# Performance work log

Measured on AMD Instinct MI355X. Metric: run time of the kernel, lower is better.

## Reference

```python
import jax, jax.numpy as jnp
import numpy as np

N_HEADS = 4
D_K = 64


def setup_inputs() -> dict:
    key = jax.random.key(0)
    k1, k2, k3, k4, k5 = jax.random.split(key, 5)
    C = 256
    return {
        "x": jax.random.normal(k1, (16, C, 32, 32), dtype=jnp.float32),
        "W_qkv": jax.random.normal(k2, (C, N_HEADS * D_K * 3), dtype=jnp.float32) * (C ** -0.5),
        "b_qkv": jax.random.normal(k3, (N_HEADS * D_K * 3,), dtype=jnp.float32) * 0.02,
        "W_out": jax.random.normal(k4, (N_HEADS * D_K, C), dtype=jnp.float32) * ((N_HEADS * D_K) ** -0.5),
        "b_out": jax.random.normal(k5, (C,), dtype=jnp.float32) * 0.02,
    }


def reference(x, W_qkv, b_qkv, W_out, b_out):
    # NOTE: the original forward never applies self.norm and ignores t.
    B, C, H, W = x.shape
    N = H * W
    scale = D_K ** -0.5
    xf = x.reshape(B, C, N).transpose(0, 2, 1)            # [B, N, C]
    qkv = (xf @ W_qkv + b_qkv).reshape(B, N, N_HEADS, 3 * D_K)
    q, k, v = jnp.split(qkv, 3, axis=-1)                  # each [B, N, H, dk]
    attn = jnp.einsum('bihd,bjhd->bijh', q, k) * scale    # [B, N, N, H]
    attn = jax.nn.softmax(attn, axis=2)                   # softmax over keys (j)
    res = jnp.einsum('bijh,bjhd->bihd', attn, v)          # [B, N, H, dk]
    res = res.reshape(B, N, N_HEADS * D_K)
    res = res @ W_out + b_out + xf                        # residual on flattened x
    return res.transpose(0, 2, 1).reshape(B, C, H, W)
```

## Files before the change

kernel.cpp:

```cpp
#include <hip/hip_runtime.h>
#include <math.h>

#define NN 1024

typedef __attribute__((ext_vector_type(8))) __bf16 bf16x8;
typedef __attribute__((ext_vector_type(4))) __bf16 bf16x4;
typedef __attribute__((ext_vector_type(4))) float f32x4;

__device__ __forceinline__ unsigned short f2bf(float f) {
    __bf16 h = (__bf16)f;
    return *(unsigned short*)&h;
}
__device__ __forceinline__ ushort4 pack4(float a, float b, float c, float d) {
    bf16x4 v;
    v[0] = (__bf16)a; v[1] = (__bf16)b; v[2] = (__bf16)c; v[3] = (__bf16)d;
    return *(ushort4*)&v;
}

__device__ __forceinline__ void async_cp16(const unsigned short* g, unsigned short* l) {
    __builtin_amdgcn_global_load_lds(
        (const __attribute__((address_space(1))) unsigned int*)g,
        (__attribute__((address_space(3))) unsigned int*)l,
        16, 0, 0);
}

__global__ __launch_bounds__(256) void prep_transpose(
    const float* __restrict__ x, const float* __restrict__ Wq,
    const float* __restrict__ Wo,
    unsigned short* __restrict__ xb, unsigned short* __restrict__ Wqt,
    unsigned short* __restrict__ Wot)
{
    __shared__ __align__(16) unsigned short T[64 * 72];
    const int bx = blockIdx.x;
    const int rt = blockIdx.y;
    const float* src; unsigned short* dst; int ncol, c0;
    if (bx < 256) {
        int b = bx >> 4; int ct = bx & 15;
        src = x + (size_t)b * 256 * 1024; dst = xb + (size_t)b * 1024 * 256;
        ncol = 1024; c0 = ct * 64;
    } else if (bx < 268) {
        src = Wq; dst = Wqt; ncol = 768; c0 = (bx - 256) * 64;
    } else {
        src = Wo; dst = Wot; ncol = 256; c0 = (bx - 268) * 64;
    }
    const int t = threadIdx.x;
    #pragma unroll
    for (int i = 0; i < 4; ++i) {
        int r  = i * 16 + (t >> 4);
        int c4 = (t & 15) * 4;
        float4 v = *(const float4*)&src[(size_t)(rt * 64 + r) * ncol + c0 + c4];
        *(ushort4*)&T[r * 72 + c4] = pack4(v.x, v.y, v.z, v.w);
    }
    __syncthreads();
    #pragma unroll
    for (int i = 0; i < 2; ++i) {
        int task = t + 256 * i;
        int c = task & 63, rs = task >> 6;
        ushort u8[8];
        #pragma unroll
        for (int k = 0; k < 8; ++k) u8[k] = T[(rs * 8 + k) * 72 + c];
        *(uint4*)&dst[(size_t)(c0 + c) * 256 + rt * 64 + rs * 8] = *(uint4*)u8;
    }
}

__global__ __launch_bounds__(256, 4) void qkv_gemm(
    const unsigned short* __restrict__ xb, const unsigned short* __restrict__ Wqt,
    const float* __restrict__ bias,
    unsigned short* __restrict__ Qb, unsigned short* __restrict__ Kb,
    unsigned short* __restrict__ Vtb)
{
    __shared__ __align__(16) unsigned short As[128 * 40];
    __shared__ __align__(16) unsigned short Bs[128 * 40];
    const int jt = blockIdx.x;
    const int m0 = blockIdx.y * 128;
    const int b  = m0 >> 10;
    const int n0 = m0 & 1023;
    const int t = threadIdx.x;
    const int w = t >> 6, lane = t & 63, quad = lane >> 4, cc = lane & 15;
    const int wm = (w & 1) * 64;
    const int wj = (w >> 1) * 64;

    f32x4 acc[4][4];
    #pragma unroll
    for (int ms = 0; ms < 4; ++ms)
        #pragma unroll
        for (int js = 0; js < 4; ++js) acc[ms][js] = (f32x4)(0.f);

    for (int k0 = 0; k0 < 256; k0 += 32) {
        __syncthreads();
        #pragma unroll
        for (int i = 0; i < 2; ++i) {
            int flat = t + 256 * i;
            int row = flat >> 2, seg = flat & 3;
            *(uint4*)&As[row * 40 + seg * 8] =
                *(const uint4*)&xb[(size_t)(m0 + row) * 256 + k0 + seg * 8];
            *(uint4*)&Bs[row * 40 + seg * 8] =
                *(const uint4*)&Wqt[(size_t)(jt * 128 + row) * 256 + k0 + seg * 8];
        }
        __syncthreads();
        bf16x8 af[4], bfr[4];
        #pragma unroll
        for (int ms = 0; ms < 4; ++ms)
            af[ms] = *(bf16x8*)&As[(wm + ms * 16 + cc) * 40 + quad * 8];
        #pragma unroll
        for (int js = 0; js < 4; ++js)
            bfr[js] = *(bf16x8*)&Bs[(wj + js * 16 + cc) * 40 + quad * 8];
        #pragma unroll
        for (int ms = 0; ms < 4; ++ms)
            #pragma unroll
            for (int js = 0; js < 4; ++js)
                acc[ms][js] = __builtin_amdgcn_mfma_f32_16x16x32_bf16(
                    af[ms], bfr[js], acc[ms][js], 0, 0, 0);
    }

    const int chunk = jt * 2 + (w >> 1);
    const int h = chunk / 3, type = chunk % 3;
    const size_t bh = (size_t)b * 4 + h;
    float bias_r[4];
    #pragma unroll
    for (int js = 0; js < 4; ++js) bias_r[js] = bias[jt * 128 + wj + js * 16 + cc];

    if (type == 2) {
        #pragma unroll
        for (int ms = 0; ms < 4; ++ms)
            #pragma unroll
            for (int js = 0; js < 4; ++js) {
                int dd = js * 16 + cc;
                int n = n0 + wm + ms * 16 + quad * 4;
                *(ushort4*)&Vtb[(bh * 64 + dd) * NN + n] =
                    pack4(acc[ms][js][0] + bias_r[js], acc[ms][js][1] + bias_r[js],
                          acc[ms][js][2] + bias_r[js], acc[ms][js][3] + bias_r[js]);
            }
    } else {
        unsigned short* dst = type ? Kb : Qb;
        const float sc = type ? 1.0f : 0.125f;
        #pragma unroll
        for (int ms = 0; ms < 4; ++ms)
            #pragma unroll
            for (int js = 0; js < 4; ++js)
                #pragma unroll
                for (int r = 0; r < 4; ++r) {
                    int n = n0 + wm + ms * 16 + quad * 4 + r;
                    dst[(bh * NN + n) * 64 + js * 16 + cc] =
                        f2bf((acc[ms][js][r] + bias_r[js]) * sc);
                }
    }
}

__global__ __launch_bounds__(256) void flash_attn(
    const unsigned short* __restrict__ Qb, const unsigned short* __restrict__ Kb,
    const unsigned short* __restrict__ Vtb, unsigned short* __restrict__ resb)
{
    __shared__ __align__(16) unsigned short Qs[4096];
    __shared__ __align__(16) unsigned short Ks0[4096];
    __shared__ __align__(16) unsigned short Ks1[4096];
    __shared__ __align__(16) unsigned short Vt0[4096];
    __shared__ __align__(16) unsigned short Vt1[4096];
    __shared__ __align__(16) unsigned short Ps[64 * 72];

    const int blk = blockIdx.x;
    const int qt = blk & 15;
    const int h  = (blk >> 4) & 3;
    const int b  = blk >> 6;
    const int t  = threadIdx.x;
    const int w  = t >> 6;
    const int lane = t & 63;
    const int quad = lane >> 4;
    const int c    = lane & 15;

    const size_t bh = (size_t)(b * 4 + h);
    const unsigned short* Qg = Qb  + bh * NN * 64;
    const unsigned short* Kg = Kb  + bh * NN * 64;
    const unsigned short* Vg = Vtb + bh * 64 * NN;

    #pragma unroll
    for (int i = 0; i < 2; ++i) {
        int f = i * 256 + t;
        int row = f >> 3;
        int gc  = (f & 7) ^ (row & 7);
        async_cp16(&Qg[(size_t)(qt * 64 + row) * 64 + gc * 8], &Qs[f * 8]);
        async_cp16(&Kg[(size_t)row * 64 + gc * 8], &Ks0[f * 8]);
        async_cp16(&Vg[(size_t)row * NN + gc * 8], &Vt0[f * 8]);
    }
    __syncthreads();

    bf16x8 qf[2];
    #pragma unroll
    for (int ks = 0; ks < 2; ++ks) {
        int sc_ = (ks * 4 + quad) ^ (c & 7);
        qf[ks] = *(bf16x8*)&Qs[((w * 16 + c) * 8 + sc_) * 8];
    }

    float m_i = -INFINITY, l_i = 0.f;
    f32x4 O[4];
    #pragma unroll
    for (int dt = 0; dt < 4; ++dt) O[dt] = (f32x4)(0.f);

    auto step = [&](int kt, const unsigned short* curK, const unsigned short* curV,
                    unsigned short* nxtK, unsigned short* nxtV,
                    bool pref, bool bar) {
        if (bar) __syncthreads();
        if (pref) {
            int ktn = kt + 1;
            #pragma unroll
            for (int i = 0; i < 2; ++i) {
                int f = i * 256 + t;
                int row = f >> 3;
                int gc  = (f & 7) ^ (row & 7);
                async_cp16(&Kg[(size_t)(ktn * 64 + row) * 64 + gc * 8], &nxtK[f * 8]);
                async_cp16(&Vg[(size_t)row * NN + ktn * 64 + gc * 8], &nxtV[f * 8]);
            }
        }

        f32x4 S[4];
        #pragma unroll
        for (int jt = 0; jt < 4; ++jt) S[jt] = (f32x4)(0.f);
        #pragma unroll
        for (int ks = 0; ks < 2; ++ks) {
            #pragma unroll
            for (int jt = 0; jt < 4; ++jt) {
                int sc_ = (ks * 4 + quad) ^ (c & 7);
                bf16x8 kf = *(bf16x8*)&curK[((jt * 16 + c) * 8 + sc_) * 8];
                S[jt] = __builtin_amdgcn_mfma_f32_16x16x32_bf16(kf, qf[ks], S[jt], 0, 0, 0);
            }
        }

        float mt = -INFINITY;
        #pragma unroll
        for (int jt = 0; jt < 4; ++jt)
            #pragma unroll
            for (int r = 0; r < 4; ++r) mt = fmaxf(mt, S[jt][r]);
        mt = fmaxf(mt, __shfl_xor(mt, 16));
        mt = fmaxf(mt, __shfl_xor(mt, 32));
        float mn = fmaxf(m_i, mt);
        float alpha = __expf(m_i - mn);
        float p[4][4];
        float rs = 0.f;
        #pragma unroll
        for (int jt = 0; jt < 4; ++jt)
            #pragma unroll
            for (int r = 0; r < 4; ++r) {
                p[jt][r] = __expf(S[jt][r] - mn);
                rs += p[jt][r];
            }
        rs += __shfl_xor(rs, 16);
        rs += __shfl_xor(rs, 32);
        l_i = l_i * alpha + rs;
        m_i = mn;

        #pragma unroll
        for (int jt = 0; jt < 4; ++jt)
            *(ushort4*)&Ps[(w * 16 + c) * 72 + jt * 16 + quad * 4] =
                pack4(p[jt][0], p[jt][1], p[jt][2], p[jt][3]);

        float alpha_r[4];
        #pragma unroll
        for (int r = 0; r < 4; ++r) alpha_r[r] = __shfl(alpha, quad * 4 + r);
        #pragma unroll
        for (int dt = 0; dt < 4; ++dt)
            #pragma unroll
            for (int r = 0; r < 4; ++r) O[dt][r] *= alpha_r[r];

        #pragma unroll
        for (int js = 0; js < 2; ++js) {
            bf16x8 pf = *(bf16x8*)&Ps[(w * 16 + c) * 72 + js * 32 + quad * 8];
            #pragma unroll
            for (int dt = 0; dt < 4; ++dt) {
                int sc_ = (js * 4 + quad) ^ (c & 7);
                bf16x8 vf = *(bf16x8*)&curV[((dt * 16 + c) * 8 + sc_) * 8];
                O[dt] = __builtin_amdgcn_mfma_f32_16x16x32_bf16(pf, vf, O[dt], 0, 0, 0);
            }
        }
    };

    step(0, Ks0, Vt0, Ks1, Vt1, true, false);
    for (int kt2 = 0; kt2 < 7; ++kt2) {
        int kt = 2 * kt2 + 1;
        step(kt,     Ks1, Vt1, Ks0, Vt0, true, true);
        step(kt + 1, Ks0, Vt0, Ks1, Vt1, true, true);
    }
    step(15, Ks1, Vt1, Ks0, Vt0, false, true);

    float linv[4];
    #pragma unroll
    for (int r = 0; r < 4; ++r) linv[r] = 1.f / __shfl(l_i, quad * 4 + r);
    #pragma unroll
    for (int dt = 0; dt < 4; ++dt)
        #pragma unroll
        for (int r = 0; r < 4; ++r) {
            int row = qt * 64 + w * 16 + quad * 4 + r;
            resb[((size_t)(b * NN + row)) * 256 + h * 64 + dt * 16 + c] =
                f2bf(O[dt][r] * linv[r]);
        }
}

__global__ __launch_bounds__(256, 4) void out_gemm(
    const unsigned short* __restrict__ resb, const unsigned short* __restrict__ Wot,
    const float* __restrict__ bias, const float* __restrict__ x,
    float* __restrict__ out)
{
    __shared__ __align__(16) unsigned short As[64 * 40];
    __shared__ __align__(16) unsigned short Bs[64 * 40];
    const int n0 = blockIdx.x * 64;
    const int c0 = blockIdx.y * 64;
    const int b  = blockIdx.z;
    const int t = threadIdx.x;
    const int w = t >> 6, lane = t & 63, quad = lane >> 4, cc = lane & 15;
    const int wm = (w & 1) * 32;
    const int wj = (w >> 1) * 32;

    f32x4 acc[2][2];
    #pragma unroll
    for (int ms = 0; ms < 2; ++ms)
        #pragma unroll
        for (int js = 0; js < 2; ++js) acc[ms][js] = (f32x4)(0.f);

    for (int k0 = 0; k0 < 256; k0 += 32) {
        __syncthreads();
        {
            int r = t >> 2, seg = t & 3;
            *(uint4*)&As[r * 40 + seg * 8] =
                *(const uint4*)&resb[((size_t)b * NN + n0 + r) * 256 + k0 + seg * 8];
            *(uint4*)&Bs[r * 40 + seg * 8] =
                *(const uint4*)&Wot[(size_t)(c0 + r) * 256 + k0 + seg * 8];
        }
        __syncthreads();
        bf16x8 af[2], bfr[2];
        #pragma unroll
        for (int ms = 0; ms < 2; ++ms)
            af[ms] = *(bf16x8*)&As[(wm + ms * 16 + cc) * 40 + quad * 8];
        #pragma unroll
        for (int js = 0; js < 2; ++js)
            bfr[js] = *(bf16x8*)&Bs[(wj + js * 16 + cc) * 40 + quad * 8];
        #pragma unroll
        for (int ms = 0; ms < 2; ++ms)
            #pragma unroll
            for (int js = 0; js < 2; ++js)
                acc[ms][js] = __builtin_amdgcn_mfma_f32_16x16x32_bf16(
                    af[ms], bfr[js], acc[ms][js], 0, 0, 0);
    }

    #pragma unroll
    for (int js = 0; js < 2; ++js) {
        int cI = c0 + wj + js * 16 + cc;
        float bi = bias[cI];
        #pragma unroll
        for (int ms = 0; ms < 2; ++ms) {
            int n = n0 + wm + ms * 16 + quad * 4;
            size_t off = ((size_t)b * 256 + cI) * NN + n;
            float4 xr = *(const float4*)&x[off];
            float4 o;
            o.x = acc[ms][js][0] + bi + xr.x;
            o.y = acc[ms][js][1] + bi + xr.y;
            o.z = acc[ms][js][2] + bi + xr.z;
            o.w = acc[ms][js][3] + bi + xr.w;
            *(float4*)&out[off] = o;
        }
    }
}

extern "C" void kernel_launch(void* const* d_in, const int* in_sizes, int n_in,
                              void* d_out, int out_size, void* d_ws, size_t ws_size,
                              hipStream_t stream)
{
    const float* x     = (const float*)d_in[0];
    const float* W_qkv = (const float*)d_in[1];
    const float* b_qkv = (const float*)d_in[2];
    const float* W_out = (const float*)d_in[3];
    const float* b_out = (const float*)d_in[4];
    float* out = (float*)d_out;

    char* wsc = (char*)d_ws;
    unsigned short* xb   = (unsigned short*)(wsc);
    unsigned short* Wqt  = (unsigned short*)(wsc + ((size_t)8 << 20));
    unsigned short* Wot  = (unsigned short*)(wsc + ((size_t)8 << 20) + ((size_t)512 << 10));
    unsigned short* Qb   = (unsigned short*)(wsc + ((size_t)9  << 20));
    unsigned short* Kb   = (unsigned short*)(wsc + ((size_t)17 << 20));
    unsigned short* Vtb  = (unsigned short*)(wsc + ((size_t)25 << 20));
    unsigned short* resb = (unsigned short*)(wsc + ((size_t)33 << 20));

    prep_transpose<<<dim3(272, 4), 256, 0, stream>>>(x, W_qkv, W_out, xb, Wqt, Wot);
    qkv_gemm<<<dim3(6, 128), 256, 0, stream>>>(xb, Wqt, b_qkv, Qb, Kb, Vtb);
    flash_attn<<<dim3(1024), 256, 0, stream>>>(Qb, Kb, Vtb, resb);
    out_gemm<<<dim3(16, 4, 16), 256, 0, stream>>>(resb, Wot, b_out, x, out);
}
```

Baseline: 146.9 us.

## Reuse Q shared buffer for P, use exp2 softmax, raise occupancy bound

```diff
diff --git a/kernel.cpp b/kernel.cpp
--- a/kernel.cpp
+++ b/kernel.cpp
@@ -133,7 +133,7 @@
             }
     } else {
         unsigned short* dst = type ? Kb : Qb;
-        const float sc = type ? 1.0f : 0.125f;
+        const float sc = type ? 1.0f : 0.18033688011112042f;
         #pragma unroll
         for (int ms = 0; ms < 4; ++ms)
             #pragma unroll
@@ -147,16 +147,15 @@
     }
 }
 
-__global__ __launch_bounds__(256) void flash_attn(
+__global__ __launch_bounds__(256, 4) void flash_attn(
     const unsigned short* __restrict__ Qb, const unsigned short* __restrict__ Kb,
     const unsigned short* __restrict__ Vtb, unsigned short* __restrict__ resb)
 {
-    __shared__ __align__(16) unsigned short Qs[4096];
+    __shared__ __align__(16) unsigned short QP[4096];
     __shared__ __align__(16) unsigned short Ks0[4096];
     __shared__ __align__(16) unsigned short Ks1[4096];
     __shared__ __align__(16) unsigned short Vt0[4096];
     __shared__ __align__(16) unsigned short Vt1[4096];
-    __shared__ __align__(16) unsigned short Ps[64 * 72];
 
     const int blk = blockIdx.x;
     const int qt = blk & 15;
@@ -178,7 +177,7 @@
         int f = i * 256 + t;
         int row = f >> 3;
         int gc  = (f & 7) ^ (row & 7);
-        async_cp16(&Qg[(size_t)(qt * 64 + row) * 64 + gc * 8], &Qs[f * 8]);
+        async_cp16(&Qg[(size_t)(qt * 64 + row) * 64 + gc * 8], &QP[f * 8]);
         async_cp16(&Kg[(size_t)row * 64 + gc * 8], &Ks0[f * 8]);
         async_cp16(&Vg[(size_t)row * NN + gc * 8], &Vt0[f * 8]);
     }
@@ -188,7 +187,7 @@
     #pragma unroll
     for (int ks = 0; ks < 2; ++ks) {
         int sc_ = (ks * 4 + quad) ^ (c & 7);
-        qf[ks] = *(bf16x8*)&Qs[((w * 16 + c) * 8 + sc_) * 8];
+        qf[ks] = *(bf16x8*)&QP[((w * 16 + c) * 8 + sc_) * 8];
     }
 
     float m_i = -INFINITY, l_i = 0.f;
@@ -225,33 +224,35 @@
             }
         }
 
-        float mt = -INFINITY;
+        float tj[4];
         #pragma unroll
         for (int jt = 0; jt < 4; ++jt)
-            #pragma unroll
-            for (int r = 0; r < 4; ++r) mt = fmaxf(mt, S[jt][r]);
+            tj[jt] = fmaxf(fmaxf(S[jt][0], S[jt][1]), fmaxf(S[jt][2], S[jt][3]));
+        float mt = fmaxf(fmaxf(tj[0], tj[1]), fmaxf(tj[2], tj[3]));
         mt = fmaxf(mt, __shfl_xor(mt, 16));
         mt = fmaxf(mt, __shfl_xor(mt, 32));
         float mn = fmaxf(m_i, mt);
-        float alpha = __expf(m_i - mn);
-        float p[4][4];
-        float rs = 0.f;
-        #pragma unroll
-        for (int jt = 0; jt < 4; ++jt)
-            #pragma unroll
-            for (int r = 0; r < 4; ++r) {
-                p[jt][r] = __expf(S[jt][r] - mn);
-                rs += p[jt][r];
-            }
+        float alpha = __builtin_amdgcn_exp2f(m_i - mn);
+        float p[4][4], rsj[4];
+        #pragma unroll
+        for (int jt = 0; jt < 4; ++jt) {
+            #pragma unroll
+            for (int r = 0; r < 4; ++r)
+                p[jt][r] = __builtin_amdgcn_exp2f(S[jt][r] - mn);
+            rsj[jt] = (p[jt][0] + p[jt][1]) + (p[jt][2] + p[jt][3]);
+        }
+        float rs = (rsj[0] + rsj[1]) + (rsj[2] + rsj[3]);
         rs += __shfl_xor(rs, 16);
         rs += __shfl_xor(rs, 32);
         l_i = l_i * alpha + rs;
         m_i = mn;
 
         #pragma unroll
-        for (int jt = 0; jt < 4; ++jt)
-            *(ushort4*)&Ps[(w * 16 + c) * 72 + jt * 16 + quad * 4] =
+        for (int jt = 0; jt < 4; ++jt) {
+            int scw = (jt * 2 + (quad >> 1)) ^ (c & 7);
+            *(ushort4*)&QP[(w * 16 + c) * 64 + scw * 8 + (quad & 1) * 4] =
                 pack4(p[jt][0], p[jt][1], p[jt][2], p[jt][3]);
+        }
 
         float alpha_r[4];
         #pragma unroll
@@ -263,7 +264,8 @@
 
         #pragma unroll
         for (int js = 0; js < 2; ++js) {
-            bf16x8 pf = *(bf16x8*)&Ps[(w * 16 + c) * 72 + js * 32 + quad * 8];
+            int scp = (js * 4 + quad) ^ (c & 7);
+            bf16x8 pf = *(bf16x8*)&QP[(w * 16 + c) * 64 + scp * 8];
             #pragma unroll
             for (int dt = 0; dt < 4; ++dt) {
                 int sc_ = (js * 4 + quad) ^ (c & 7);
```

Result: faster. 138.0 us (-6.1%).
